# Kernel optimization log

Measured on AMD Instinct MI355X. Metric: run time of the kernel, lower is better.

The kernel has to match this reference:

```python
import jax, jax.numpy as jnp
import numpy as np
from jax import lax

RADII = (0.1, 0.2, 0.4)
NBRS = (16, 32, 64)
PE_DIM = 24
CENTER_PE_DIM = 96
EPS = 1e-5


def sinusoidal_3d(x, dim):
    # x: [..., 3] -> [..., dim]; dim//3 features per axis (half sin, half cos)
    per_axis = dim // 3
    half = per_axis // 2
    freq = jnp.exp(-jnp.log(10000.0) * jnp.arange(half, dtype=x.dtype) / (half - 1))
    ang = x[..., None] * freq                      # [..., 3, half]
    emb = jnp.concatenate([jnp.sin(ang), jnp.cos(ang)], axis=-1)  # [..., 3, per_axis]
    return emb.reshape(x.shape[:-1] + (dim,))


def layer_norm(x, g, b):
    m = jnp.mean(x, axis=-1, keepdims=True)
    v = jnp.var(x, axis=-1, keepdims=True)
    return (x - m) * lax.rsqrt(v + EPS) * g + b


def point_mlp(x, W, b, g, beta, act):
    y = layer_norm(x @ W + b, g, beta)
    return jax.nn.gelu(y, approximate=False) if act else y


def index_points(pts, idx):
    # pts: [B,N,C], idx: [B,...] -> [B,...,C]
    bidx = jnp.arange(pts.shape[0]).reshape((-1,) + (1,) * (idx.ndim - 1))
    return pts[bidx, idx]


def farthest_point_sample(xyz, npoint):
    # xyz: [B,N,3] -> idx [B,npoint]
    N = xyz.shape[1]

    def single(pts):
        def step(carry, _):
            dist, far = carry
            c = pts[far]                                   # [3]
            d = jnp.sum((pts - c) ** 2, axis=-1)           # [N]
            dist = jnp.minimum(dist, d)
            nxt = jnp.argmax(dist).astype(jnp.int32)
            return (dist, nxt), far
        init = (jnp.full((N,), 1e10, pts.dtype), jnp.int32(0))
        _, idxs = lax.scan(step, init, None, length=npoint)
        return idxs

    return jax.vmap(single)(xyz)


def query_ball_point(radius, k, xyz, centers):
    # xyz: [B,N,3], centers: [B,S,3] -> [B,S,k] neighbor indices
    N = xyz.shape[1]
    sqr = jnp.sum((centers[:, :, None, :] - xyz[:, None, :, :]) ** 2, axis=-1)  # [B,S,N]
    gidx = jnp.where(sqr > radius * radius, N, jnp.arange(N)[None, None, :])
    gidx = jnp.sort(gidx, axis=-1)[..., :k]
    first = gidx[..., :1]
    return jnp.where(gidx == N, first, gidx)


def setup_inputs() -> dict:
    key = jax.random.key(0)
    ks = jax.random.split(key, 8)
    B, N, STEM, TOK = 16, 4096, 128, 256
    d_in = STEM + 3 + PE_DIM          # 155
    d_tok_in = STEM + 3 * TOK + CENTER_PE_DIM  # 992
    sc = 0.02
    return {
        "xyz": jax.random.uniform(ks[0], (B, N, 3), dtype=jnp.float32),
        "point_feature": jax.random.normal(ks[1], (B, N, STEM), dtype=jnp.float32) * 0.1,
        "sW1": jax.random.normal(ks[2], (3, d_in, TOK), dtype=jnp.float32) * sc,
        "sb1": jnp.zeros((3, TOK)), "sg1": jnp.ones((3, TOK)), "sbeta1": jnp.zeros((3, TOK)),
        "sW2": jax.random.normal(ks[3], (3, TOK, TOK), dtype=jnp.float32) * sc,
        "sb2": jnp.zeros((3, TOK)), "sg2": jnp.ones((3, TOK)), "sbeta2": jnp.zeros((3, TOK)),
        "tW1": jax.random.normal(ks[4], (d_tok_in, TOK), dtype=jnp.float32) * sc,
        "tb1": jnp.zeros((TOK,)), "tg1": jnp.ones((TOK,)), "tbeta1": jnp.zeros((TOK,)),
        "tW2": jax.random.normal(ks[5], (TOK, TOK), dtype=jnp.float32) * sc,
        "tb2": jnp.zeros((TOK,)), "tg2": jnp.ones((TOK,)), "tbeta2": jnp.zeros((TOK,)),
    }


def reference(xyz, point_feature, sW1, sb1, sg1, sbeta1, sW2, sb2, sg2, sbeta2,
              tW1, tb1, tg1, tbeta1, tW2, tb2, tg2, tbeta2):
    S = 512  # num_patches
    center_idx = farthest_point_sample(xyz, S)            # [B,S]
    patch_center = index_points(xyz, center_idx)          # [B,S,3]
    center_feature = index_points(point_feature, center_idx)  # [B,S,STEM]

    scale_feats = []
    for s, (r, k) in enumerate(zip(RADII, NBRS)):
        nidx = query_ball_point(r, k, xyz, patch_center)  # [B,S,k]
        gxyz = index_points(xyz, nidx)                    # [B,S,k,3]
        gfeat = index_points(point_feature, nidx)         # [B,S,k,STEM]
        rel = gxyz - patch_center[:, :, None, :]
        rel_pe = sinusoidal_3d(rel, PE_DIM)
        gin = jnp.concatenate([gfeat, rel, rel_pe], axis=-1)   # [B,S,k,155]
        h = point_mlp(gin, sW1[s], sb1[s], sg1[s], sbeta1[s], True)
        h = point_mlp(h, sW2[s], sb2[s], sg2[s], sbeta2[s], False)
        scale_feats.append(jnp.max(h, axis=2))            # [B,S,TOK]

    center_pe = sinusoidal_3d(patch_center, CENTER_PE_DIM)    # [B,S,96]
    tok_in = jnp.concatenate([center_feature] + scale_feats + [center_pe], axis=-1)
    tok = point_mlp(tok_in, tW1, tb1, tg1, tbeta1, True)
    tok = point_mlp(tok, tW2, tb2, tg2, tbeta2, False)
    return tok, patch_center
```

## Files before the change

### kernel.cpp

```cpp
#include <hip/hip_runtime.h>
#include <math.h>

#define BATCH 16
#define NPTS  4096
#define NCTR  512
#define STEM  128
#define TOK   256
#define D_IN  155
#define D_TOK 992

typedef short s16x8 __attribute__((ext_vector_type(8)));
typedef float f32x4 __attribute__((ext_vector_type(4)));

static constexpr float FR15c[16] = {
    1.0f, 0.5411695265464638f, 0.2928644487857941f, 0.15848931670188904f,
    0.08576958626508713f, 0.04641588851809502f, 0.02511886507272720f, 0.01359356392547488f,
    0.007356422487646341f, 0.003981071710586548f, 0.002154434798285365f, 0.001165914465673268f,
    0.0006309573450125754f, 0.0003414548910222948f, 0.0001847849769866168f, 0.0001f};

__device__ __forceinline__ unsigned short f2bf(float f) {
    unsigned u = __float_as_uint(f);
    u += 0x7FFF + ((u >> 16) & 1);
    return (unsigned short)(u >> 16);
}
// ... 38 lines not shown
    float t = __builtin_amdgcn_rcpf(fmaf(0.3275911f, a, 1.0f));
    float p = fmaf(1.061405429f, t, -1.453152027f);
    p = fmaf(p, t, 1.421413741f);
    p = fmaf(p, t, -0.284496736f);
    p = fmaf(p, t, 0.254829592f);
    p = p * t;
    float e = __expf(-z * z);
    float y = fmaf(-p, e, 1.0f);
    y = (z < 0.0f) ? -y : y;
    return 0.5f * x * (1.0f + y);
}

__device__ __forceinline__ float sq3(float ax, float ay, float az,
                                     float bx, float by, float bz) {
    float dx = __fsub_rn(ax, bx);
    float dy = __fsub_rn(ay, by);
    float dz = __fsub_rn(az, bz);
    float d = __fmul_rn(dx, dx);
    d = __fadd_rn(d, __fmul_rn(dy, dy));
    d = __fadd_rn(d, __fmul_rn(dz, dz));
    return d;
}

__global__ __launch_bounds__(256) void fps_kernel(const float* __restrict__ xyz,
                                                  int* __restrict__ center_idx,
                                                  float* __restrict__ pc_ws,
                                                  float* __restrict__ pc_out) {
    int b = blockIdx.x;
    int t = threadIdx.x;
    const int w = t >> 6, lane = t & 63;
    const float* X = xyz + (size_t)b * NPTS * 3;
    __shared__ __align__(16) float sxyz[NPTS * 3];
    __shared__ float swv[2][4];
    __shared__ int   swi[2][4];
    __shared__ int   hist[NCTR];
    {
        const float4* src = (const float4*)X;
        float4* dst = (float4*)sxyz;
        for (int i = t; i < NPTS * 3 / 4; i += 256) dst[i] = src[i];
    }
    __syncthreads();
    float px[16], py[16], pz[16], dist[16];
#pragma unroll
    for (int j = 0; j < 16; ++j) {
        int i = t + 256 * j;
        px[j] = sxyz[i * 3 + 0];
        py[j] = sxyz[i * 3 + 1];
        pz[j] = sxyz[i * 3 + 2];
        dist[j] = 1e10f;
    }
    int far = 0;
    for (int s = 0; s < NCTR; ++s) {
        if (t == 0) hist[s] = far;
        float cx = sxyz[far * 3 + 0];
        float cy = sxyz[far * 3 + 1];
        float cz = sxyz[far * 3 + 2];
        float bv = -1.0f;
        int bi = 0;
#pragma unroll
        for (int j = 0; j < 16; ++j) {
            float d = sq3(px[j], py[j], pz[j], cx, cy, cz);
            float nd = fminf(dist[j], d);
            dist[j] = nd;
            if (nd > bv) { bv = nd; bi = t + 256 * j; }
        }
#pragma unroll
        for (int off = 32; off >= 1; off >>= 1) {
            float ov = __shfl_xor(bv, off, 64);
            int   oi = __shfl_xor(bi, off, 64);
            if (ov > bv || (ov == bv && oi < bi)) { bv = ov; bi = oi; }
        }
        const int p = s & 1;
        if (lane == 0) { swv[p][w] = bv; swi[p][w] = bi; }
        __syncthreads();
        bv = swv[p][0]; bi = swi[p][0];
#pragma unroll
        for (int ww = 1; ww < 4; ++ww) {
            float ov = swv[p][ww]; int oi = swi[p][ww];
            if (ov > bv || (ov == bv && oi < bi)) { bv = ov; bi = oi; }
        }
        far = bi;
    }
    __syncthreads();
    for (int s = t; s < NCTR; s += 256) {
        int idx = hist[s];
        center_idx[b * NCTR + s] = idx;
        float cx = sxyz[idx * 3], cy = sxyz[idx * 3 + 1], cz = sxyz[idx * 3 + 2];
        size_t po = (size_t)(b * NCTR + s) * 3;
        pc_ws[po] = cx; pc_ws[po + 1] = cy; pc_ws[po + 2] = cz;
        pc_out[po] = cx; pc_out[po + 1] = cy; pc_out[po + 2] = cz;
    }
}

template <int K>
__global__ __launch_bounds__(256) void ballq_kernel(const float* __restrict__ xyz,
                                                    const float* __restrict__ pc,
                                                    int* __restrict__ nbr,
                                                    float rr) {
    int cid = blockIdx.x * 4 + (threadIdx.x >> 6);
    int lane = threadIdx.x & 63;
    int b = cid >> 9;
    const float* X = xyz + (size_t)b * NPTS * 3;
    float cx = pc[(size_t)cid * 3 + 0];
    float cy = pc[(size_t)cid * 3 + 1];
    float cz = pc[(size_t)cid * 3 + 2];
    int cnt = 0, first = 0;
    bool have_first = false;
    long long base = (long long)cid * K;
    for (int it = 0; it < NPTS / 64; ++it) {
        int i = it * 64 + lane;
        float d = sq3(cx, cy, cz, X[i * 3], X[i * 3 + 1], X[i * 3 + 2]);
        bool ok = d <= rr;
        unsigned long long mask = __ballot(ok);
        if (!have_first && mask) {
            first = it * 64 + (int)__builtin_ctzll(mask);
            have_first = true;
        }
        int pos = cnt + (int)__popcll(mask & ((1ull << lane) - 1ull));
        if (ok && pos < K) nbr[base + pos] = i;
        cnt += (int)__popcll(mask);
        if (cnt >= K) break;
    }
    int fill = cnt < K ? cnt : K;
    for (int j = fill + lane; j < K; j += 64) nbr[base + j] = first;
}

__global__ __launch_bounds__(256) void pack_w(const float* __restrict__ Wbase,
                                              unsigned short* __restrict__ out,
                                              int Kdim, int KS) {
    int s = blockIdx.y;
    const float* W = Wbase + (size_t)s * Kdim * TOK;
    unsigned short* o = out + (size_t)s * 16 * KS * 64 * 16;
    int tid = blockIdx.x * 256 + threadIdx.x;
    if (tid >= 16 * KS * 64) return;
    int lane = tid & 63;
    int frag = tid >> 6;
    int ks = frag % KS;
    int ct = frag / KS;
    int col = ct * 16 + (lane & 15);
    int k0 = ks * 32 + (lane >> 4) * 8;
    unsigned short* hi = o + (size_t)frag * 1024 + lane * 8;
    unsigned short* lo = hi + 512;
#pragma unroll
    for (int j = 0; j < 8; ++j) {
        int k = k0 + j;
        float v = (k < Kdim) ? W[(size_t)k * TOK + col] : 0.0f;
        unsigned short h = f2bf(v);
        hi[j] = h;
        lo[j] = f2bf(v - bf2f(h));
    }
}

template <int K>
__global__ __launch_bounds__(256, 2) void scale_mfma(
    const float* __restrict__ xyz, const float* __restrict__ pf,
    const unsigned short* __restrict__ pk1, const float* __restrict__ b1,
    const float* __restrict__ g1, const float* __restrict__ be1,
    const unsigned short* __restrict__ pk2, const float* __restrict__ b2,
    const float* __restrict__ g2, const float* __restrict__ be2,
    const int* __restrict__ nbr, const float* __restrict__ pc,
    float* __restrict__ outf) {
    __shared__ unsigned int hpk[64][260];
    __shared__ float lnred[4][64][2];
    const int w = threadIdx.x >> 6, l = threadIdx.x & 63;
    const int lg = l >> 4, li = l & 15;
    const int ws4 = 4 * w;

    int nb[4];
    float relx[4], rely[4], relz[4];
#pragma unroll
    for (int rb = 0; rb < 4; ++rb) {
        int row_g = blockIdx.x * 64 + rb * 16 + li;
        int c = (blockIdx.x * 64 + rb * 16) / K;
        int b = c >> 9;
        int n = nbr[row_g];
        nb[rb] = b * NPTS + n;
        const float* X = xyz + (size_t)nb[rb] * 3;
        const float* C = pc + (size_t)c * 3;
        relx[rb] = __fsub_rn(X[0], C[0]);
        rely[rb] = __fsub_rn(X[1], C[1]);
        relz[rb] = __fsub_rn(X[2], C[2]);
    }

    f32x4 acc1[4][4];
#pragma unroll
    for (int rb = 0; rb < 4; ++rb)
#pragma unroll
        for (int ctl = 0; ctl < 4; ++ctl) acc1[rb][ctl] = (f32x4){0.f, 0.f, 0.f, 0.f};

#pragma unroll
    for (int ks = 0; ks < 5; ++ks) {
        s16x8 Bh[4], Bl[4];
#pragma unroll
        for (int ctl = 0; ctl < 4; ++ctl)
            loadB(pk1, (ws4 + ctl) * 5 + ks, l, Bh[ctl], Bl[ctl]);
        s16x8 Ah[4], Al[4];
#pragma unroll
        for (int rb = 0; rb < 4; ++rb) {
            float v[8];
            if (ks < 4) {
                const float* src = pf + (size_t)nb[rb] * STEM + ks * 32 + lg * 8;
                float4 f0 = *(const float4*)src;
                float4 f1 = *(const float4*)(src + 4);
                v[0] = f0.x; v[1] = f0.y; v[2] = f0.z; v[3] = f0.w;
                v[4] = f1.x; v[5] = f1.y; v[6] = f1.z; v[7] = f1.w;
            } else {
#pragma unroll
                for (int j = 0; j < 8; ++j) {
                    int ch = lg * 8 + j;
                    float val = 0.0f;
                    if (ch < 3) {
                        val = (ch == 0) ? relx[rb] : ((ch == 1) ? rely[rb] : relz[rb]);
                    } else if (ch < 27) {
                        int rem = ch - 3;
                        int axis = rem >> 3, r8 = rem & 7;
                        int fi = (r8 < 4) ? r8 : r8 - 4;
                        float fr = (fi == 0) ? 1.0f
                                  : (fi == 1) ? 0.046415888336127795f
                                  : (fi == 2) ? 0.0021544346900318843f : 1e-4f;
                        float rl = (axis == 0) ? relx[rb] : ((axis == 1) ? rely[rb] : relz[rb]);
                        float ang = rl * fr;
                        val = (r8 < 4) ? __sinf(ang) : __cosf(ang);
                    }
                    v[j] = val;
                }
            }
            bsplit8(v, Ah[rb], Al[rb]);
        }
#pragma unroll
        for (int ctl = 0; ctl < 4; ++ctl)
#pragma unroll
            for (int rb = 0; rb < 4; ++rb) {
                acc1[rb][ctl] = __builtin_amdgcn_mfma_f32_16x16x32_bf16(Ah[rb], Bh[ctl], acc1[rb][ctl], 0, 0, 0);
                acc1[rb][ctl] = __builtin_amdgcn_mfma_f32_16x16x32_bf16(Ah[rb], Bl[ctl], acc1[rb][ctl], 0, 0, 0);
                acc1[rb][ctl] = __builtin_amdgcn_mfma_f32_16x16x32_bf16(Al[rb], Bh[ctl], acc1[rb][ctl], 0, 0, 0);
            }
    }

    {
        float b1v[4], g1v[4], be1v[4];
#pragma unroll
        for (int ctl = 0; ctl < 4; ++ctl) {
            int col = w * 64 + ctl * 16 + li;
            b1v[ctl] = b1[col]; g1v[ctl] = g1[col]; be1v[ctl] = be1[col];
        }
#pragma unroll
        for (int rb = 0; rb < 4; ++rb)
#pragma unroll
            for (int reg = 0; reg < 4; ++reg) {
                float s = 0.f, ss = 0.f;
#pragma unroll
                for (int ctl = 0; ctl < 4; ++ctl) {
                    float x = acc1[rb][ctl][reg] + b1v[ctl];
                    s += x; ss = fmaf(x, x, ss);
                }
#pragma unroll
                for (int m = 1; m <= 8; m <<= 1) {
                    s += __shfl_xor(s, m, 64);
                    ss += __shfl_xor(ss, m, 64);
                }
                if (li == 0) {
                    lnred[w][rb * 16 + lg * 4 + reg][0] = s;
                    lnred[w][rb * 16 + lg * 4 + reg][1] = ss;
                }
            }
        __syncthreads();
#pragma unroll
        for (int rb = 0; rb < 4; ++rb)
#pragma unroll
            for (int reg = 0; reg < 4; ++reg) {
                int row = rb * 16 + lg * 4 + reg;
                float s = lnred[0][row][0] + lnred[1][row][0] + lnred[2][row][0] + lnred[3][row][0];
                float ss = lnred[0][row][1] + lnred[1][row][1] + lnred[2][row][1] + lnred[3][row][1];
                float mean = s * (1.0f / 256.0f);
                float var = ss * (1.0f / 256.0f) - mean * mean;
                float rs = rsqrtf(var + 1e-5f);
#pragma unroll
                for (int ctl = 0; ctl < 4; ++ctl) {
                    float x = acc1[rb][ctl][reg] + b1v[ctl];
                    acc1[rb][ctl][reg] = gelu_exact((x - mean) * rs * g1v[ctl] + be1v[ctl]);
                }
            }
    }

#pragma unroll
    for (int rb = 0; rb < 4; ++rb)
#pragma unroll
        for (int ctl = 0; ctl < 4; ++ctl) {
            unsigned w0, w1, w2, w3;
            pkpair(acc1[rb][ctl][0], acc1[rb][ctl][1], w0, w1);
            pkpair(acc1[rb][ctl][2], acc1[rb][ctl][3], w2, w3);
            int r0 = rb * 16 + lg * 4;
            int kc = w * 64 + ctl * 16 + li;
            hpk[r0 + 0][kc] = w0; hpk[r0 + 1][kc] = w1;
            hpk[r0 + 2][kc] = w2; hpk[r0 + 3][kc] = w3;
        }
    __syncthreads();

    f32x4 acc2[4][4];
#pragma unroll
    for (int rb = 0; rb < 4; ++rb)
#pragma unroll
        for (int ctl = 0; ctl < 4; ++ctl) acc2[rb][ctl] = (f32x4){0.f, 0.f, 0.f, 0.f};

#pragma unroll
    for (int q = 0; q < 8; ++q) {
        s16x8 Bh[4], Bl[4];
#pragma unroll
        for (int ctl = 0; ctl < 4; ++ctl)
            loadB(pk2, (ws4 + ctl) * 8 + q, l, Bh[ctl], Bl[ctl]);
#pragma unroll
        for (int rb = 0; rb < 4; ++rb) {
            const unsigned int* hp = &hpk[rb * 16 + li][q * 32 + lg * 8];
            int4 xa = *(const int4*)hp;
            int4 xb = *(const int4*)(hp + 4);
            unsigned x[8] = {(unsigned)xa.x, (unsigned)xa.y, (unsigned)xa.z, (unsigned)xa.w,
                             (unsigned)xb.x, (unsigned)xb.y, (unsigned)xb.z, (unsigned)xb.w};
            union { s16x8 s; unsigned w[4]; } H, L;
#pragma unroll
            for (int p = 0; p < 4; ++p) {
                H.w[p] = (x[2 * p] >> 16) | (x[2 * p + 1] & 0xffff0000u);
                L.w[p] = (x[2 * p] & 0xffffu) | (x[2 * p + 1] << 16);
            }
#pragma unroll
            for (int ctl = 0; ctl < 4; ++ctl) {
                acc2[rb][ctl] = __builtin_amdgcn_mfma_f32_16x16x32_bf16(H.s, Bh[ctl], acc2[rb][ctl], 0, 0, 0);
                acc2[rb][ctl] = __builtin_amdgcn_mfma_f32_16x16x32_bf16(H.s, Bl[ctl], acc2[rb][ctl], 0, 0, 0);
                acc2[rb][ctl] = __builtin_amdgcn_mfma_f32_16x16x32_bf16(L.s, Bh[ctl], acc2[rb][ctl], 0, 0, 0);
            }
        }
    }

    float b2v[4], g2v[4], be2v[4];
#pragma unroll
    for (int ctl = 0; ctl < 4; ++ctl) {
        int col = w * 64 + ctl * 16 + li;
        b2v[ctl] = b2[col]; g2v[ctl] = g2[col]; be2v[ctl] = be2[col];
    }
#pragma unroll
    for (int rb = 0; rb < 4; ++rb)
#pragma unroll
        for (int reg = 0; reg < 4; ++reg) {
            float s = 0.f, ss = 0.f;
#pragma unroll
            for (int ctl = 0; ctl < 4; ++ctl) {
                float x = acc2[rb][ctl][reg] + b2v[ctl];
                s += x; ss = fmaf(x, x, ss);
            }
#pragma unroll
            for (int m = 1; m <= 8; m <<= 1) {
                s += __shfl_xor(s, m, 64);
                ss += __shfl_xor(ss, m, 64);
            }
            if (li == 0) {
                lnred[w][rb * 16 + lg * 4 + reg][0] = s;
                lnred[w][rb * 16 + lg * 4 + reg][1] = ss;
            }
        }
    __syncthreads();
#pragma unroll
    for (int rb = 0; rb < 4; ++rb)
#pragma unroll
        for (int reg = 0; reg < 4; ++reg) {
            int row = rb * 16 + lg * 4 + reg;
            float s = lnred[0][row][0] + lnred[1][row][0] + lnred[2][row][0] + lnred[3][row][0];
            float ss = lnred[0][row][1] + lnred[1][row][1] + lnred[2][row][1] + lnred[3][row][1];
            float mean = s * (1.0f / 256.0f);
            float var = ss * (1.0f / 256.0f) - mean * mean;
            float rs = rsqrtf(var + 1e-5f);
#pragma unroll
            for (int ctl = 0; ctl < 4; ++ctl) {
                float x = acc2[rb][ctl][reg] + b2v[ctl];
                acc2[rb][ctl][reg] = (x - mean) * rs * g2v[ctl] + be2v[ctl];
            }
        }

    const int CPB = 64 / K;
    const int RBC = K / 16;
#pragma unroll
    for (int cg = 0; cg < CPB; ++cg)
#pragma unroll
        for (int ctl = 0; ctl < 4; ++ctl) {
            float mx = -3.4e38f;
#pragma unroll
            for (int rbl = 0; rbl < RBC; ++rbl) {
                int rb = cg * RBC + rbl;
#pragma unroll
                for (int reg = 0; reg < 4; ++reg) mx = fmaxf(mx, acc2[rb][ctl][reg]);
            }
            mx = fmaxf(mx, __shfl_xor(mx, 16, 64));
            mx = fmaxf(mx, __shfl_xor(mx, 32, 64));
            if (lg == 0)
                outf[(size_t)(blockIdx.x * CPB + cg) * TOK + w * 64 + ctl * 16 + li] = mx;
        }
}

__global__ __launch_bounds__(256, 2) void token_mfma(
    const float* __restrict__ pf, const int* __restrict__ center_idx,
    const float* __restrict__ pc, const float* __restrict__ sf0,
    const float* __restrict__ sf1, const float* __restrict__ sf2,
    const unsigned short* __restrict__ pk1, const float* __restrict__ b1,
    const float* __restrict__ g1, const float* __restrict__ be1,
    const unsigned short* __restrict__ pk2, const float* __restrict__ b2,
    const float* __restrict__ g2, const float* __restrict__ be2,
    float* __restrict__ out) {
    __shared__ unsigned int hpk[32][260];
    __shared__ float lnred[4][32][2];
    const int w = threadIdx.x >> 6, l = threadIdx.x & 63;
    const int lg = l >> 4, li = l & 15;
    const int ws4 = 4 * w;
    const int rowbase = blockIdx.x * 32;

    int rowg[2];
    const float* pfc[2];
    float pcx[2], pcy[2], pcz[2];
#pragma unroll
    for (int rb = 0; rb < 2; ++rb) {
        int row = rowbase + rb * 16 + li;
        rowg[rb] = row;
        int b = row >> 9;
        int cidx = center_idx[row];
        pfc[rb] = pf + ((size_t)b * NPTS + cidx) * STEM;
        pcx[rb] = pc[(size_t)row * 3 + 0];
        pcy[rb] = pc[(size_t)row * 3 + 1];
        pcz[rb] = pc[(size_t)row * 3 + 2];
    }

    f32x4 acc1[2][4];
#pragma unroll
    for (int rb = 0; rb < 2; ++rb)
#pragma unroll
        for (int ctl = 0; ctl < 4; ++ctl) acc1[rb][ctl] = (f32x4){0.f, 0.f, 0.f, 0.f};

#pragma unroll 2
    for (int ks = 0; ks < 31; ++ks) {
        s16x8 Bh[4], Bl[4];
#pragma unroll
        for (int ctl = 0; ctl < 4; ++ctl)
            loadB(pk1, (ws4 + ctl) * 31 + ks, l, Bh[ctl], Bl[ctl]);
        s16x8 Ah[2], Al[2];
#pragma unroll
        for (int rb = 0; rb < 2; ++rb) {
            float v[8];
            if (ks < 28) {
                const float* src;
                if (ks < 4)       src = pfc[rb] + ks * 32 + lg * 8;
                else if (ks < 12) src = sf0 + (size_t)rowg[rb] * TOK + (ks - 4) * 32 + lg * 8;
                else if (ks < 20) src = sf1 + (size_t)rowg[rb] * TOK + (ks - 12) * 32 + lg * 8;
                else              src = sf2 + (size_t)rowg[rb] * TOK + (ks - 20) * 32 + lg * 8;
                float4 f0 = *(const float4*)src;
                float4 f1 = *(const float4*)(src + 4);
                v[0] = f0.x; v[1] = f0.y; v[2] = f0.z; v[3] = f0.w;
                v[4] = f1.x; v[5] = f1.y; v[6] = f1.z; v[7] = f1.w;
            } else {
                float c = (ks == 28) ? pcx[rb] : ((ks == 29) ? pcy[rb] : pcz[rb]);
#pragma unroll
                for (int j = 0; j < 8; ++j) {
                    float fr = (lg & 1) ? FR15c[8 + j] : FR15c[j];
                    float ang = c * fr;
                    v[j] = (lg < 2) ? __sinf(ang) : __cosf(ang);
                }
            }
            bsplit8(v, Ah[rb], Al[rb]);
        }
#pragma unroll
        for (int ctl = 0; ctl < 4; ++ctl)
#pragma unroll
            for (int rb = 0; rb < 2; ++rb) {
                acc1[rb][ctl] = __builtin_amdgcn_mfma_f32_16x16x32_bf16(Ah[rb], Bh[ctl], acc1[rb][ctl], 0, 0, 0);
                acc1[rb][ctl] = __builtin_amdgcn_mfma_f32_16x16x32_bf16(Ah[rb], Bl[ctl], acc1[rb][ctl], 0, 0, 0);
                acc1[rb][ctl] = __builtin_amdgcn_mfma_f32_16x16x32_bf16(Al[rb], Bh[ctl], acc1[rb][ctl], 0, 0, 0);
            }
    }

    {
        float b1v[4], g1v[4], be1v[4];
#pragma unroll
        for (int ctl = 0; ctl < 4; ++ctl) {
            int col = w * 64 + ctl * 16 + li;
            b1v[ctl] = b1[col]; g1v[ctl] = g1[col]; be1v[ctl] = be1[col];
        }
#pragma unroll
        for (int rb = 0; rb < 2; ++rb)
#pragma unroll
            for (int reg = 0; reg < 4; ++reg) {
                float s = 0.f, ss = 0.f;
#pragma unroll
                for (int ctl = 0; ctl < 4; ++ctl) {
                    float x = acc1[rb][ctl][reg] + b1v[ctl];
                    s += x; ss = fmaf(x, x, ss);
                }
#pragma unroll
                for (int m = 1; m <= 8; m <<= 1) {
                    s += __shfl_xor(s, m, 64);
                    ss += __shfl_xor(ss, m, 64);
                }
                if (li == 0) {
                    lnred[w][rb * 16 + lg * 4 + reg][0] = s;
                    lnred[w][rb * 16 + lg * 4 + reg][1] = ss;
                }
            }
        __syncthreads();
#pragma unroll
        for (int rb = 0; rb < 2; ++rb)
#pragma unroll
            for (int reg = 0; reg < 4; ++reg) {
                int row = rb * 16 + lg * 4 + reg;
                float s = lnred[0][row][0] + lnred[1][row][0] + lnred[2][row][0] + lnred[3][row][0];
                float ss = lnred[0][row][1] + lnred[1][row][1] + lnred[2][row][1] + lnred[3][row][1];
                float mean = s * (1.0f / 256.0f);
                float var = ss * (1.0f / 256.0f) - mean * mean;
                float rs = rsqrtf(var + 1e-5f);
#pragma unroll
                for (int ctl = 0; ctl < 4; ++ctl) {
                    float x = acc1[rb][ctl][reg] + b1v[ctl];
                    acc1[rb][ctl][reg] = gelu_exact((x - mean) * rs * g1v[ctl] + be1v[ctl]);
                }
            }
    }

#pragma unroll
    for (int rb = 0; rb < 2; ++rb)
#pragma unroll
        for (int ctl = 0; ctl < 4; ++ctl) {
            unsigned w0, w1, w2, w3;
            pkpair(acc1[rb][ctl][0], acc1[rb][ctl][1], w0, w1);
            pkpair(acc1[rb][ctl][2], acc1[rb][ctl][3], w2, w3);
            int r0 = rb * 16 + lg * 4;
            int kc = w * 64 + ctl * 16 + li;
            hpk[r0 + 0][kc] = w0; hpk[r0 + 1][kc] = w1;
            hpk[r0 + 2][kc] = w2; hpk[r0 + 3][kc] = w3;
        }
    __syncthreads();

    f32x4 acc2[2][4];
#pragma unroll
    for (int rb = 0; rb < 2; ++rb)
#pragma unroll
        for (int ctl = 0; ctl < 4; ++ctl) acc2[rb][ctl] = (f32x4){0.f, 0.f, 0.f, 0.f};
#pragma unroll
    for (int q = 0; q < 8; ++q) {
        s16x8 Bh[4], Bl[4];
#pragma unroll
        for (int ctl = 0; ctl < 4; ++ctl)
            loadB(pk2, (ws4 + ctl) * 8 + q, l, Bh[ctl], Bl[ctl]);
#pragma unroll
        for (int rb = 0; rb < 2; ++rb) {
            const unsigned int* hp = &hpk[rb * 16 + li][q * 32 + lg * 8];
            int4 xa = *(const int4*)hp;
            int4 xb = *(const int4*)(hp + 4);
            unsigned x[8] = {(unsigned)xa.x, (unsigned)xa.y, (unsigned)xa.z, (unsigned)xa.w,
                             (unsigned)xb.x, (unsigned)xb.y, (unsigned)xb.z, (unsigned)xb.w};
            union { s16x8 s; unsigned w[4]; } H, L;
#pragma unroll
            for (int p = 0; p < 4; ++p) {
                H.w[p] = (x[2 * p] >> 16) | (x[2 * p + 1] & 0xffff0000u);
                L.w[p] = (x[2 * p] & 0xffffu) | (x[2 * p + 1] << 16);
            }
#pragma unroll
            for (int ctl = 0; ctl < 4; ++ctl) {
                acc2[rb][ctl] = __builtin_amdgcn_mfma_f32_16x16x32_bf16(H.s, Bh[ctl], acc2[rb][ctl], 0, 0, 0);
                acc2[rb][ctl] = __builtin_amdgcn_mfma_f32_16x16x32_bf16(H.s, Bl[ctl], acc2[rb][ctl], 0, 0, 0);
                acc2[rb][ctl] = __builtin_amdgcn_mfma_f32_16x16x32_bf16(L.s, Bh[ctl], acc2[rb][ctl], 0, 0, 0);
            }
        }
    }

    float b2v[4], g2v[4], be2v[4];
#pragma unroll
    for (int ctl = 0; ctl < 4; ++ctl) {
        int col = w * 64 + ctl * 16 + li;
        b2v[ctl] = b2[col]; g2v[ctl] = g2[col]; be2v[ctl] = be2[col];
    }
#pragma unroll
    for (int rb = 0; rb < 2; ++rb)
#pragma unroll
        for (int reg = 0; reg < 4; ++reg) {
            float s = 0.f, ss = 0.f;
#pragma unroll
            for (int ctl = 0; ctl < 4; ++ctl) {
                float x = acc2[rb][ctl][reg] + b2v[ctl];
                s += x; ss = fmaf(x, x, ss);
            }
#pragma unroll
            for (int m = 1; m <= 8; m <<= 1) {
                s += __shfl_xor(s, m, 64);
                ss += __shfl_xor(ss, m, 64);
            }
            if (li == 0) {
                lnred[w][rb * 16 + lg * 4 + reg][0] = s;
                lnred[w][rb * 16 + lg * 4 + reg][1] = ss;
            }
        }
    __syncthreads();
#pragma unroll
    for (int rb = 0; rb < 2; ++rb)
#pragma unroll
        for (int reg = 0; reg < 4; ++reg) {
            int row = rb * 16 + lg * 4 + reg;
            float s = lnred[0][row][0] + lnred[1][row][0] + lnred[2][row][0] + lnred[3][row][0];
            float ss = lnred[0][row][1] + lnred[1][row][1] + lnred[2][row][1] + lnred[3][row][1];
            float mean = s * (1.0f / 256.0f);
            float var = ss * (1.0f / 256.0f) - mean * mean;
            float rs = rsqrtf(var + 1e-5f);
#pragma unroll
            for (int ctl = 0; ctl < 4; ++ctl) {
                float x = acc2[rb][ctl][reg] + b2v[ctl];
                float v = (x - mean) * rs * g2v[ctl] + be2v[ctl];
                out[(size_t)(rowbase + row) * TOK + w * 64 + ctl * 16 + li] = v;
            }
        }
}

extern "C" void kernel_launch(void* const* d_in, const int* in_sizes, int n_in,
                              void* d_out, int out_size, void* d_ws, size_t ws_size,
                              hipStream_t stream) {
    const float* xyz  = (const float*)d_in[0];
    const float* pf   = (const float*)d_in[1];
    const float* sW1  = (const float*)d_in[2];
    const float* sb1  = (const float*)d_in[3];
    const float* sg1  = (const float*)d_in[4];
    const float* sbe1 = (const float*)d_in[5];
    const float* sW2  = (const float*)d_in[6];
    const float* sb2  = (const float*)d_in[7];
    const float* sg2  = (const float*)d_in[8];
    const float* sbe2 = (const float*)d_in[9];
    const float* tW1  = (const float*)d_in[10];
    const float* tb1  = (const float*)d_in[11];
    const float* tg1  = (const float*)d_in[12];
    const float* tbe1 = (const float*)d_in[13];
    const float* tW2  = (const float*)d_in[14];
    const float* tb2  = (const float*)d_in[15];
    const float* tg2  = (const float*)d_in[16];
    const float* tbe2 = (const float*)d_in[17];

    float* out_tok = (float*)d_out;
    float* out_pc  = out_tok + (size_t)BATCH * NCTR * TOK;

    char* ws = (char*)d_ws;
    int* center_idx = (int*)ws;   ws += (size_t)BATCH * NCTR * 4;
    float* pc_ws    = (float*)ws; ws += (size_t)BATCH * NCTR * 3 * 4;
    int* nbr0       = (int*)ws;   ws += (size_t)BATCH * NCTR * 16 * 4;
    int* nbr1       = (int*)ws;   ws += (size_t)BATCH * NCTR * 32 * 4;
    int* nbr2       = (int*)ws;   ws += (size_t)BATCH * NCTR * 64 * 4;
    float* sf0      = (float*)ws; ws += (size_t)BATCH * NCTR * TOK * 4;
    float* sf1      = (float*)ws; ws += (size_t)BATCH * NCTR * TOK * 4;
    float* sf2      = (float*)ws; ws += (size_t)BATCH * NCTR * TOK * 4;
    const size_t PK1_S  = 16 * 5 * 64 * 16;
    const size_t PK2_S  = 16 * 8 * 64 * 16;
    const size_t PKT1_S = 16 * 31 * 64 * 16;
    const size_t PKT2_S = 16 * 8 * 64 * 16;
    unsigned short* pkW1 = (unsigned short*)ws; ws += 3 * PK1_S * 2;
    unsigned short* pkW2 = (unsigned short*)ws; ws += 3 * PK2_S * 2;
    unsigned short* pkT1 = (unsigned short*)ws; ws += PKT1_S * 2;
    unsigned short* pkT2 = (unsigned short*)ws; ws += PKT2_S * 2;

    {
        dim3 gp1((16 * 5 * 64 + 255) / 256, 3);
        pack_w<<<gp1, 256, 0, stream>>>(sW1, pkW1, D_IN, 5);
        dim3 gp2((16 * 8 * 64 + 255) / 256, 3);
        pack_w<<<gp2, 256, 0, stream>>>(sW2, pkW2, TOK, 8);
        dim3 gpt1((16 * 31 * 64 + 255) / 256, 1);
        pack_w<<<gpt1, 256, 0, stream>>>(tW1, pkT1, D_TOK, 31);
        dim3 gpt2((16 * 8 * 64 + 255) / 256, 1);
        pack_w<<<gpt2, 256, 0, stream>>>(tW2, pkT2, TOK, 8);
    }

    fps_kernel<<<BATCH, 256, 0, stream>>>(xyz, center_idx, pc_ws, out_pc);

    ballq_kernel<16><<<BATCH * NCTR / 4, 256, 0, stream>>>(xyz, pc_ws, nbr0, (float)(0.1 * 0.1));
    ballq_kernel<32><<<BATCH * NCTR / 4, 256, 0, stream>>>(xyz, pc_ws, nbr1, (float)(0.2 * 0.2));
    ballq_kernel<64><<<BATCH * NCTR / 4, 256, 0, stream>>>(xyz, pc_ws, nbr2, (float)(0.4 * 0.4));

    scale_mfma<16><<<(BATCH * NCTR * 16) / 64, 256, 0, stream>>>(
        xyz, pf, pkW1 + 0 * PK1_S, sb1 + 0 * TOK, sg1 + 0 * TOK, sbe1 + 0 * TOK,
        pkW2 + 0 * PK2_S, sb2 + 0 * TOK, sg2 + 0 * TOK, sbe2 + 0 * TOK,
        nbr0, pc_ws, sf0);
    scale_mfma<32><<<(BATCH * NCTR * 32) / 64, 256, 0, stream>>>(
        xyz, pf, pkW1 + 1 * PK1_S, sb1 + 1 * TOK, sg1 + 1 * TOK, sbe1 + 1 * TOK,
        pkW2 + 1 * PK2_S, sb2 + 1 * TOK, sg2 + 1 * TOK, sbe2 + 1 * TOK,
        nbr1, pc_ws, sf1);
    scale_mfma<64><<<(BATCH * NCTR * 64) / 64, 256, 0, stream>>>(
        xyz, pf, pkW1 + 2 * PK1_S, sb1 + 2 * TOK, sg1 + 2 * TOK, sbe1 + 2 * TOK,
        pkW2 + 2 * PK2_S, sb2 + 2 * TOK, sg2 + 2 * TOK, sbe2 + 2 * TOK,
        nbr2, pc_ws, sf2);

    token_mfma<<<(BATCH * NCTR) / 32, 256, 0, stream>>>(
        pf, center_idx, pc_ws, sf0, sf1, sf2,
        pkT1, tb1, tg1, tbe1, pkT2, tb2, tg2, tbe2, out_tok);
}
```

Baseline: 1.634 ms.

## Split second GEMM into half-row passes, swizzle LDS, shrink token blocks

The scale kernel now runs its second GEMM and LayerNorm in two passes of 32 rows each. This halves the LDS staging buffer and the acc2 register footprint, and the staging buffer uses an XOR swizzle instead of row padding. Max-pooling is done per pass, with a running max carried across passes for K=64. Launch bounds rise to 3 blocks per CU to raise occupancy. The token kernel drops to 16 rows per block with double the grid, trading weight reuse for lower register and LDS use and more parallelism.

```diff
diff --git a/kernel.cpp b/kernel.cpp
--- a/kernel.cpp
+++ b/kernel.cpp
@@ -214,7 +214,7 @@
 }
 
 template <int K>
-__global__ __launch_bounds__(256, 2) void scale_mfma(
+__global__ __launch_bounds__(256, 3) void scale_mfma(
     const float* __restrict__ xyz, const float* __restrict__ pf,
     const unsigned short* __restrict__ pk1, const float* __restrict__ b1,
     const float* __restrict__ g1, const float* __restrict__ be1,
@@ -222,7 +222,7 @@
     const float* __restrict__ g2, const float* __restrict__ be2,
     const int* __restrict__ nbr, const float* __restrict__ pc,
     float* __restrict__ outf) {
-    __shared__ unsigned int hpk[64][260];
+    __shared__ unsigned int hpk[32 * 256];
     __shared__ float lnred[4][64][2];
     const int w = threadIdx.x >> 6, l = threadIdx.x & 63;
     const int lg = l >> 4, li = l & 15;
@@ -345,119 +345,160 @@
             }
     }
 
-#pragma unroll
-    for (int rb = 0; rb < 4; ++rb)
-#pragma unroll
-        for (int ctl = 0; ctl < 4; ++ctl) {
-            unsigned w0, w1, w2, w3;
-            pkpair(acc1[rb][ctl][0], acc1[rb][ctl][1], w0, w1);
-            pkpair(acc1[rb][ctl][2], acc1[rb][ctl][3], w2, w3);
-            int r0 = rb * 16 + lg * 4;
-            int kc = w * 64 + ctl * 16 + li;
-            hpk[r0 + 0][kc] = w0; hpk[r0 + 1][kc] = w1;
-            hpk[r0 + 2][kc] = w2; hpk[r0 + 3][kc] = w3;
-        }
-    __syncthreads();
-
-    f32x4 acc2[4][4];
-#pragma unroll
-    for (int rb = 0; rb < 4; ++rb)
-#pragma unroll
-        for (int ctl = 0; ctl < 4; ++ctl) acc2[rb][ctl] = (f32x4){0.f, 0.f, 0.f, 0.f};
-
-#pragma unroll
-    for (int q = 0; q < 8; ++q) {
-        s16x8 Bh[4], Bl[4];
-#pragma unroll
-        for (int ctl = 0; ctl < 4; ++ctl)
-            loadB(pk2, (ws4 + ctl) * 8 + q, l, Bh[ctl], Bl[ctl]);
-#pragma unroll
-        for (int rb = 0; rb < 4; ++rb) {
-            const unsigned int* hp = &hpk[rb * 16 + li][q * 32 + lg * 8];
-            int4 xa = *(const int4*)hp;
-            int4 xb = *(const int4*)(hp + 4);
-            unsigned x[8] = {(unsigned)xa.x, (unsigned)xa.y, (unsigned)xa.z, (unsigned)xa.w,
-                             (unsigned)xb.x, (unsigned)xb.y, (unsigned)xb.z, (unsigned)xb.w};
-            union { s16x8 s; unsigned w[4]; } H, L;
-#pragma unroll
-            for (int p = 0; p < 4; ++p) {
-                H.w[p] = (x[2 * p] >> 16) | (x[2 * p + 1] & 0xffff0000u);
-                L.w[p] = (x[2 * p] & 0xffffu) | (x[2 * p + 1] << 16);
-            }
-#pragma unroll
-            for (int ctl = 0; ctl < 4; ++ctl) {
-                acc2[rb][ctl] = __builtin_amdgcn_mfma_f32_16x16x32_bf16(H.s, Bh[ctl], acc2[rb][ctl], 0, 0, 0);
-                acc2[rb][ctl] = __builtin_amdgcn_mfma_f32_16x16x32_bf16(H.s, Bl[ctl], acc2[rb][ctl], 0, 0, 0);
-                acc2[rb][ctl] = __builtin_amdgcn_mfma_f32_16x16x32_bf16(L.s, Bh[ctl], acc2[rb][ctl], 0, 0, 0);
-            }
-        }
-    }
-
     float b2v[4], g2v[4], be2v[4];
 #pragma unroll
     for (int ctl = 0; ctl < 4; ++ctl) {
         int col = w * 64 + ctl * 16 + li;
         b2v[ctl] = b2[col]; g2v[ctl] = g2[col]; be2v[ctl] = be2[col];
     }
-#pragma unroll
-    for (int rb = 0; rb < 4; ++rb)
-#pragma unroll
-        for (int reg = 0; reg < 4; ++reg) {
-            float s = 0.f, ss = 0.f;
+    float mx64[4];
+#pragma unroll
+    for (int ctl = 0; ctl < 4; ++ctl) mx64[ctl] = -3.4e38f;
+
+#pragma unroll
+    for (int p = 0; p < 2; ++p) {
+#pragma unroll
+        for (int rbl = 0; rbl < 2; ++rbl) {
+            const int rb = 2 * p + rbl;
 #pragma unroll
             for (int ctl = 0; ctl < 4; ++ctl) {
-                float x = acc2[rb][ctl][reg] + b2v[ctl];
-                s += x; ss = fmaf(x, x, ss);
-            }
-#pragma unroll
-            for (int m = 1; m <= 8; m <<= 1) {
-                s += __shfl_xor(s, m, 64);
-                ss += __shfl_xor(ss, m, 64);
-            }
-            if (li == 0) {
-                lnred[w][rb * 16 + lg * 4 + reg][0] = s;
-                lnred[w][rb * 16 + lg * 4 + reg][1] = ss;
-            }
-        }
-    __syncthreads();
-#pragma unroll
-    for (int rb = 0; rb < 4; ++rb)
-#pragma unroll
-        for (int reg = 0; reg < 4; ++reg) {
-            int row = rb * 16 + lg * 4 + reg;
-            float s = lnred[0][row][0] + lnred[1][row][0] + lnred[2][row][0] + lnred[3][row][0];
-            float ss = lnred[0][row][1] + lnred[1][row][1] + lnred[2][row][1] + lnred[3][row][1];
-            float mean = s * (1.0f / 256.0f);
-            float var = ss * (1.0f / 256.0f) - mean * mean;
-            float rs = rsqrtf(var + 1e-5f);
+                unsigned w0, w1, w2, w3;
+                pkpair(acc1[rb][ctl][0], acc1[rb][ctl][1], w0, w1);
+                pkpair(acc1[rb][ctl][2], acc1[rb][ctl][3], w2, w3);
+                const int lr0 = rbl * 16 + lg * 4;
+                const int kc = w * 64 + ctl * 16 + li;
+                hpk[(lr0 + 0) * 256 + (kc ^ (((lr0 + 0) & 7) << 2))] = w0;
+                hpk[(lr0 + 1) * 256 + (kc ^ (((lr0 + 1) & 7) << 2))] = w1;
+                hpk[(lr0 + 2) * 256 + (kc ^ (((lr0 + 2) & 7) << 2))] = w2;
+                hpk[(lr0 + 3) * 256 + (kc ^ (((lr0 + 3) & 7) << 2))] = w3;
+            }
+        }
+        __syncthreads();
+
+        f32x4 acc2[2][4];
+#pragma unroll
+        for (int rbl = 0; rbl < 2; ++rbl)
+#pragma unroll
+            for (int ctl = 0; ctl < 4; ++ctl) acc2[rbl][ctl] = (f32x4){0.f, 0.f, 0.f, 0.f};
+
+#pragma unroll
+        for (int q = 0; q < 8; ++q) {
+            s16x8 Bh[4], Bl[4];
+#pragma unroll
+            for (int ctl = 0; ctl < 4; ++ctl)
+                loadB(pk2, (ws4 + ctl) * 8 + q, l, Bh[ctl], Bl[ctl]);
+#pragma unroll
+            for (int rbl = 0; rbl < 2; ++rbl) {
+                const int lr = rbl * 16 + li;
+                const int sw = (lr & 7) << 2;
+                const unsigned* base = hpk + lr * 256;
+                int4 xa = *(const int4*)(base + ((q * 32 + lg * 8) ^ sw));
+                int4 xb = *(const int4*)(base + ((q * 32 + lg * 8 + 4) ^ sw));
+                unsigned x[8] = {(unsigned)xa.x, (unsigned)xa.y, (unsigned)xa.z, (unsigned)xa.w,
+                                 (unsigned)xb.x, (unsigned)xb.y, (unsigned)xb.z, (unsigned)xb.w};
+                union { s16x8 s; unsigned w[4]; } H, L;
+#pragma unroll
+                for (int pp = 0; pp < 4; ++pp) {
+                    H.w[pp] = (x[2 * pp] >> 16) | (x[2 * pp + 1] & 0xffff0000u);
+                    L.w[pp] = (x[2 * pp] & 0xffffu) | (x[2 * pp + 1] << 16);
+                }
+#pragma unroll
+                for (int ctl = 0; ctl < 4; ++ctl) {
+                    acc2[rbl][ctl] = __builtin_amdgcn_mfma_f32_16x16x32_bf16(H.s, Bh[ctl], acc2[rbl][ctl], 0, 0, 0);
+                    acc2[rbl][ctl] = __builtin_amdgcn_mfma_f32_16x16x32_bf16(H.s, Bl[ctl], acc2[rbl][ctl], 0, 0, 0);
+                    acc2[rbl][ctl] = __builtin_amdgcn_mfma_f32_16x16x32_bf16(L.s, Bh[ctl], acc2[rbl][ctl], 0, 0, 0);
+                }
+            }
+        }
+
+#pragma unroll
+        for (int rbl = 0; rbl < 2; ++rbl)
+#pragma unroll
+            for (int reg = 0; reg < 4; ++reg) {
+                float s = 0.f, ss = 0.f;
+#pragma unroll
+                for (int ctl = 0; ctl < 4; ++ctl) {
+                    float x = acc2[rbl][ctl][reg] + b2v[ctl];
+                    s += x; ss = fmaf(x, x, ss);
+                }
+#pragma unroll
+                for (int m = 1; m <= 8; m <<= 1) {
+                    s += __shfl_xor(s, m, 64);
+                    ss += __shfl_xor(ss, m, 64);
+                }
+                if (li == 0) {
+                    lnred[w][rbl * 16 + lg * 4 + reg][0] = s;
+                    lnred[w][rbl * 16 + lg * 4 + reg][1] = ss;
+                }
+            }
+        __syncthreads();
+
+#pragma unroll
+        for (int rbl = 0; rbl < 2; ++rbl)
+#pragma unroll
+            for (int reg = 0; reg < 4; ++reg) {
+                int row = rbl * 16 + lg * 4 + reg;
+                float s = lnred[0][row][0] + lnred[1][row][0] + lnred[2][row][0] + lnred[3][row][0];
+                float ss = lnred[0][row][1] + lnred[1][row][1] + lnred[2][row][1] + lnred[3][row][1];
+                float mean = s * (1.0f / 256.0f);
+                float var = ss * (1.0f / 256.0f) - mean * mean;
+                float rs = rsqrtf(var + 1e-5f);
+#pragma unroll
+                for (int ctl = 0; ctl < 4; ++ctl) {
+                    float x = acc2[rbl][ctl][reg] + b2v[ctl];
+                    acc2[rbl][ctl][reg] = (x - mean) * rs * g2v[ctl] + be2v[ctl];
+                }
+            }
+
+        if (K == 64) {
+#pragma unroll
+            for (int rbl = 0; rbl < 2; ++rbl)
+#pragma unroll
+                for (int ctl = 0; ctl < 4; ++ctl)
+#pragma unroll
+                    for (int reg = 0; reg < 4; ++reg)
+                        mx64[ctl] = fmaxf(mx64[ctl], acc2[rbl][ctl][reg]);
+        } else if (K == 32) {
 #pragma unroll
             for (int ctl = 0; ctl < 4; ++ctl) {
-                float x = acc2[rb][ctl][reg] + b2v[ctl];
-                acc2[rb][ctl][reg] = (x - mean) * rs * g2v[ctl] + be2v[ctl];
-            }
-        }
-
-    const int CPB = 64 / K;
-    const int RBC = K / 16;
-#pragma unroll
-    for (int cg = 0; cg < CPB; ++cg)
+                float mx = -3.4e38f;
+#pragma unroll
+                for (int rbl = 0; rbl < 2; ++rbl)
+#pragma unroll
+                    for (int reg = 0; reg < 4; ++reg) mx = fmaxf(mx, acc2[rbl][ctl][reg]);
+                mx = fmaxf(mx, __shfl_xor(mx, 16, 64));
+                mx = fmaxf(mx, __shfl_xor(mx, 32, 64));
+                if (lg == 0)
+                    outf[(size_t)(blockIdx.x * 2 + p) * TOK + w * 64 + ctl * 16 + li] = mx;
+            }
+        } else {
+#pragma unroll
+            for (int rbl = 0; rbl < 2; ++rbl)
+#pragma unroll
+                for (int ctl = 0; ctl < 4; ++ctl) {
+                    float mx = -3.4e38f;
+#pragma unroll
+                    for (int reg = 0; reg < 4; ++reg) mx = fmaxf(mx, acc2[rbl][ctl][reg]);
+                    mx = fmaxf(mx, __shfl_xor(mx, 16, 64));
+                    mx = fmaxf(mx, __shfl_xor(mx, 32, 64));
+                    if (lg == 0)
+                        outf[(size_t)(blockIdx.x * 4 + 2 * p + rbl) * TOK + w * 64 + ctl * 16 + li] = mx;
+                }
+        }
+    }
+    if (K == 64) {
 #pragma unroll
         for (int ctl = 0; ctl < 4; ++ctl) {
-            float mx = -3.4e38f;
-#pragma unroll
-            for (int rbl = 0; rbl < RBC; ++rbl) {
-                int rb = cg * RBC + rbl;
-#pragma unroll
-                for (int reg = 0; reg < 4; ++reg) mx = fmaxf(mx, acc2[rb][ctl][reg]);
-            }
+            float mx = mx64[ctl];
             mx = fmaxf(mx, __shfl_xor(mx, 16, 64));
             mx = fmaxf(mx, __shfl_xor(mx, 32, 64));
             if (lg == 0)
-                outf[(size_t)(blockIdx.x * CPB + cg) * TOK + w * 64 + ctl * 16 + li] = mx;
-        }
-}
-
-__global__ __launch_bounds__(256, 2) void token_mfma(
+                outf[(size_t)blockIdx.x * TOK + w * 64 + ctl * 16 + li] = mx;
+        }
+    }
+}
+
+__global__ __launch_bounds__(256, 3) void token_mfma(
     const float* __restrict__ pf, const int* __restrict__ center_idx,
     const float* __restrict__ pc, const float* __restrict__ sf0,
     const float* __restrict__ sf1, const float* __restrict__ sf2,
@@ -466,33 +507,24 @@
     const unsigned short* __restrict__ pk2, const float* __restrict__ b2,
     const float* __restrict__ g2, const float* __restrict__ be2,
     float* __restrict__ out) {
-    __shared__ unsigned int hpk[32][260];
-    __shared__ float lnred[4][32][2];
+    __shared__ unsigned int hpk[16][260];
+    __shared__ float lnred[4][16][2];
     const int w = threadIdx.x >> 6, l = threadIdx.x & 63;
     const int lg = l >> 4, li = l & 15;
     const int ws4 = 4 * w;
-    const int rowbase = blockIdx.x * 32;
-
-    int rowg[2];
-    const float* pfc[2];
-    float pcx[2], pcy[2], pcz[2];
-#pragma unroll
-    for (int rb = 0; rb < 2; ++rb) {
-        int row = rowbase + rb * 16 + li;
-        rowg[rb] = row;
-        int b = row >> 9;
-        int cidx = center_idx[row];
-        pfc[rb] = pf + ((size_t)b * NPTS + cidx) * STEM;
-        pcx[rb] = pc[(size_t)row * 3 + 0];
-        pcy[rb] = pc[(size_t)row * 3 + 1];
-        pcz[rb] = pc[(size_t)row * 3 + 2];
-    }
-
-    f32x4 acc1[2][4];
-#pragma unroll
-    for (int rb = 0; rb < 2; ++rb)
-#pragma unroll
-        for (int ctl = 0; ctl < 4; ++ctl) acc1[rb][ctl] = (f32x4){0.f, 0.f, 0.f, 0.f};
+    const int rowbase = blockIdx.x * 16;
+
+    const int rowg = rowbase + li;
+    const int bb = rowg >> 9;
+    const int cidx = center_idx[rowg];
+    const float* pfc = pf + ((size_t)bb * NPTS + cidx) * STEM;
+    const float pcx = pc[(size_t)rowg * 3 + 0];
+    const float pcy = pc[(size_t)rowg * 3 + 1];
+    const float pcz = pc[(size_t)rowg * 3 + 2];
+
+    f32x4 acc1[4];
+#pragma unroll
+    for (int ctl = 0; ctl < 4; ++ctl) acc1[ctl] = (f32x4){0.f, 0.f, 0.f, 0.f};
 
 #pragma unroll 2
     for (int ks = 0; ks < 31; ++ks) {
@@ -500,22 +532,21 @@
 #pragma unroll
         for (int ctl = 0; ctl < 4; ++ctl)
             loadB(pk1, (ws4 + ctl) * 31 + ks, l, Bh[ctl], Bl[ctl]);
-        s16x8 Ah[2], Al[2];
-#pragma unroll
-        for (int rb = 0; rb < 2; ++rb) {
+        s16x8 Ah, Al;
+        {
             float v[8];
             if (ks < 28) {
                 const float* src;
-                if (ks < 4)       src = pfc[rb] + ks * 32 + lg * 8;
-                else if (ks < 12) src = sf0 + (size_t)rowg[rb] * TOK + (ks - 4) * 32 + lg * 8;
-                else if (ks < 20) src = sf1 + (size_t)rowg[rb] * TOK + (ks - 12) * 32 + lg * 8;
-                else              src = sf2 + (size_t)rowg[rb] * TOK + (ks - 20) * 32 + lg * 8;
+                if (ks < 4)       src = pfc + ks * 32 + lg * 8;
+                else if (ks < 12) src = sf0 + (size_t)rowg * TOK + (ks - 4) * 32 + lg * 8;
+                else if (ks < 20) src = sf1 + (size_t)rowg * TOK + (ks - 12) * 32 + lg * 8;
+                else              src = sf2 + (size_t)rowg * TOK + (ks - 20) * 32 + lg * 8;
                 float4 f0 = *(const float4*)src;
                 float4 f1 = *(const float4*)(src + 4);
                 v[0] = f0.x; v[1] = f0.y; v[2] = f0.z; v[3] = f0.w;
                 v[4] = f1.x; v[5] = f1.y; v[6] = f1.z; v[7] = f1.w;
             } else {
-                float c = (ks == 28) ? pcx[rb] : ((ks == 29) ? pcy[rb] : pcz[rb]);
+                float c = (ks == 28) ? pcx : ((ks == 29) ? pcy : pcz);
 #pragma unroll
                 for (int j = 0; j < 8; ++j) {
                     float fr = (lg & 1) ? FR15c[8 + j] : FR15c[j];
@@ -523,16 +554,14 @@
                     v[j] = (lg < 2) ? __sinf(ang) : __cosf(ang);
                 }
             }
-            bsplit8(v, Ah[rb], Al[rb]);
-        }
-#pragma unroll
-        for (int ctl = 0; ctl < 4; ++ctl)
-#pragma unroll
-            for (int rb = 0; rb < 2; ++rb) {
-                acc1[rb][ctl] = __builtin_amdgcn_mfma_f32_16x16x32_bf16(Ah[rb], Bh[ctl], acc1[rb][ctl], 0, 0, 0);
-                acc1[rb][ctl] = __builtin_amdgcn_mfma_f32_16x16x32_bf16(Ah[rb], Bl[ctl], acc1[rb][ctl], 0, 0, 0);
-                acc1[rb][ctl] = __builtin_amdgcn_mfma_f32_16x16x32_bf16(Al[rb], Bh[ctl], acc1[rb][ctl], 0, 0, 0);
-            }
+            bsplit8(v, Ah, Al);
+        }
+#pragma unroll
+        for (int ctl = 0; ctl < 4; ++ctl) {
+            acc1[ctl] = __builtin_amdgcn_mfma_f32_16x16x32_bf16(Ah, Bh[ctl], acc1[ctl], 0, 0, 0);
+            acc1[ctl] = __builtin_amdgcn_mfma_f32_16x16x32_bf16(Ah, Bl[ctl], acc1[ctl], 0, 0, 0);
+            acc1[ctl] = __builtin_amdgcn_mfma_f32_16x16x32_bf16(Al, Bh[ctl], acc1[ctl], 0, 0, 0);
+        }
     }
 
     {
@@ -543,105 +572,11 @@
             b1v[ctl] = b1[col]; g1v[ctl] = g1[col]; be1v[ctl] = be1[col];
         }
 #pragma unroll
-        for (int rb = 0; rb < 2; ++rb)
-#pragma unroll
-            for (int reg = 0; reg < 4; ++reg) {
-                float s = 0.f, ss = 0.f;
-#pragma unroll
-                for (int ctl = 0; ctl < 4; ++ctl) {
-                    float x = acc1[rb][ctl][reg] + b1v[ctl];
-                    s += x; ss = fmaf(x, x, ss);
-                }
-#pragma unroll
-                for (int m = 1; m <= 8; m <<= 1) {
-                    s += __shfl_xor(s, m, 64);
-                    ss += __shfl_xor(ss, m, 64);
-                }
-                if (li == 0) {
-                    lnred[w][rb * 16 + lg * 4 + reg][0] = s;
-                    lnred[w][rb * 16 + lg * 4 + reg][1] = ss;
-                }
-            }
-        __syncthreads();
-#pragma unroll
-        for (int rb = 0; rb < 2; ++rb)
-#pragma unroll
-            for (int reg = 0; reg < 4; ++reg) {
-                int row = rb * 16 + lg * 4 + reg;
-                float s = lnred[0][row][0] + lnred[1][row][0] + lnred[2][row][0] + lnred[3][row][0];
-                float ss = lnred[0][row][1] + lnred[1][row][1] + lnred[2][row][1] + lnred[3][row][1];
-                float mean = s * (1.0f / 256.0f);
-                float var = ss * (1.0f / 256.0f) - mean * mean;
-                float rs = rsqrtf(var + 1e-5f);
-#pragma unroll
-                for (int ctl = 0; ctl < 4; ++ctl) {
-                    float x = acc1[rb][ctl][reg] + b1v[ctl];
-                    acc1[rb][ctl][reg] = gelu_exact((x - mean) * rs * g1v[ctl] + be1v[ctl]);
-                }
-            }
-    }
-
-#pragma unroll
-    for (int rb = 0; rb < 2; ++rb)
-#pragma unroll
-        for (int ctl = 0; ctl < 4; ++ctl) {
-            unsigned w0, w1, w2, w3;
-            pkpair(acc1[rb][ctl][0], acc1[rb][ctl][1], w0, w1);
-            pkpair(acc1[rb][ctl][2], acc1[rb][ctl][3], w2, w3);
-            int r0 = rb * 16 + lg * 4;
-            int kc = w * 64 + ctl * 16 + li;
-            hpk[r0 + 0][kc] = w0; hpk[r0 + 1][kc] = w1;
-            hpk[r0 + 2][kc] = w2; hpk[r0 + 3][kc] = w3;
-        }
-    __syncthreads();
-
-    f32x4 acc2[2][4];
-#pragma unroll
-    for (int rb = 0; rb < 2; ++rb)
-#pragma unroll
-        for (int ctl = 0; ctl < 4; ++ctl) acc2[rb][ctl] = (f32x4){0.f, 0.f, 0.f, 0.f};
-#pragma unroll
-    for (int q = 0; q < 8; ++q) {
-        s16x8 Bh[4], Bl[4];
-#pragma unroll
-        for (int ctl = 0; ctl < 4; ++ctl)
-            loadB(pk2, (ws4 + ctl) * 8 + q, l, Bh[ctl], Bl[ctl]);
-#pragma unroll
-        for (int rb = 0; rb < 2; ++rb) {
-            const unsigned int* hp = &hpk[rb * 16 + li][q * 32 + lg * 8];
-            int4 xa = *(const int4*)hp;
-            int4 xb = *(const int4*)(hp + 4);
-            unsigned x[8] = {(unsigned)xa.x, (unsigned)xa.y, (unsigned)xa.z, (unsigned)xa.w,
-                             (unsigned)xb.x, (unsigned)xb.y, (unsigned)xb.z, (unsigned)xb.w};
-            union { s16x8 s; unsigned w[4]; } H, L;
-#pragma unroll
-            for (int p = 0; p < 4; ++p) {
-                H.w[p] = (x[2 * p] >> 16) | (x[2 * p + 1] & 0xffff0000u);
-                L.w[p] = (x[2 * p] & 0xffffu) | (x[2 * p + 1] << 16);
-            }
-#pragma unroll
-            for (int ctl = 0; ctl < 4; ++ctl) {
-                acc2[rb][ctl] = __builtin_amdgcn_mfma_f32_16x16x32_bf16(H.s, Bh[ctl], acc2[rb][ctl], 0, 0, 0);
-                acc2[rb][ctl] = __builtin_amdgcn_mfma_f32_16x16x32_bf16(H.s, Bl[ctl], acc2[rb][ctl], 0, 0, 0);
-                acc2[rb][ctl] = __builtin_amdgcn_mfma_f32_16x16x32_bf16(L.s, Bh[ctl], acc2[rb][ctl], 0, 0, 0);
-            }
-        }
-    }
-
-    float b2v[4], g2v[4], be2v[4];
-#pragma unroll
-    for (int ctl = 0; ctl < 4; ++ctl) {
-        int col = w * 64 + ctl * 16 + li;
-        b2v[ctl] = b2[col]; g2v[ctl] = g2[col]; be2v[ctl] = be2[col];
-    }
-#pragma unroll
-    for (int rb = 0; rb < 2; ++rb)
-#pragma unroll
         for (int reg = 0; reg < 4; ++reg) {
             float s = 0.f, ss = 0.f;
 #pragma unroll
             for (int ctl = 0; ctl < 4; ++ctl) {
-                float x = acc2[rb][ctl][reg] + b2v[ctl];
+                float x = acc1[ctl][reg] + b1v[ctl];
                 s += x; ss = fmaf(x, x, ss);
             }
 #pragma unroll
@@ -650,16 +585,14 @@
                 ss += __shfl_xor(ss, m, 64);
             }
             if (li == 0) {
-                lnred[w][rb * 16 + lg * 4 + reg][0] = s;
-                lnred[w][rb * 16 + lg * 4 + reg][1] = ss;
-            }
-        }
-    __syncthreads();
-#pragma unroll
-    for (int rb = 0; rb < 2; ++rb)
+                lnred[w][lg * 4 + reg][0] = s;
+                lnred[w][lg * 4 + reg][1] = ss;
+            }
+        }
+        __syncthreads();
 #pragma unroll
         for (int reg = 0; reg < 4; ++reg) {
-            int row = rb * 16 + lg * 4 + reg;
+            int row = lg * 4 + reg;
             float s = lnred[0][row][0] + lnred[1][row][0] + lnred[2][row][0] + lnred[3][row][0];
             float ss = lnred[0][row][1] + lnred[1][row][1] + lnred[2][row][1] + lnred[3][row][1];
             float mean = s * (1.0f / 256.0f);
@@ -667,11 +600,92 @@
             float rs = rsqrtf(var + 1e-5f);
 #pragma unroll
             for (int ctl = 0; ctl < 4; ++ctl) {
-                float x = acc2[rb][ctl][reg] + b2v[ctl];
-                float v = (x - mean) * rs * g2v[ctl] + be2v[ctl];
-                out[(size_t)(rowbase + row) * TOK + w * 64 + ctl * 16 + li] = v;
-            }
-        }
+                float x = acc1[ctl][reg] + b1v[ctl];
+                acc1[ctl][reg] = gelu_exact((x - mean) * rs * g1v[ctl] + be1v[ctl]);
+            }
+        }
+    }
+
+#pragma unroll
+    for (int ctl = 0; ctl < 4; ++ctl) {
+        unsigned w0, w1, w2, w3;
+        pkpair(acc1[ctl][0], acc1[ctl][1], w0, w1);
+        pkpair(acc1[ctl][2], acc1[ctl][3], w2, w3);
+        int r0 = lg * 4;
+        int kc = w * 64 + ctl * 16 + li;
+        hpk[r0 + 0][kc] = w0; hpk[r0 + 1][kc] = w1;
+        hpk[r0 + 2][kc] = w2; hpk[r0 + 3][kc] = w3;
+    }
+    __syncthreads();
+
+    f32x4 acc2[4];
+#pragma unroll
+    for (int ctl = 0; ctl < 4; ++ctl) acc2[ctl] = (f32x4){0.f, 0.f, 0.f, 0.f};
+#pragma unroll
+    for (int q = 0; q < 8; ++q) {
+        s16x8 Bh[4], Bl[4];
+#pragma unroll
+        for (int ctl = 0; ctl < 4; ++ctl)
+            loadB(pk2, (ws4 + ctl) * 8 + q, l, Bh[ctl], Bl[ctl]);
+        const unsigned int* hp = &hpk[li][q * 32 + lg * 8];
+        int4 xa = *(const int4*)hp;
+        int4 xb = *(const int4*)(hp + 4);
+        unsigned x[8] = {(unsigned)xa.x, (unsigned)xa.y, (unsigned)xa.z, (unsigned)xa.w,
+                         (unsigned)xb.x, (unsigned)xb.y, (unsigned)xb.z, (unsigned)xb.w};
+        union { s16x8 s; unsigned w[4]; } H, L;
+#pragma unroll
+        for (int pp = 0; pp < 4; ++pp) {
+            H.w[pp] = (x[2 * pp] >> 16) | (x[2 * pp + 1] & 0xffff0000u);
+            L.w[pp] = (x[2 * pp] & 0xffffu) | (x[2 * pp + 1] << 16);
+        }
+#pragma unroll
+        for (int ctl = 0; ctl < 4; ++ctl) {
+            acc2[ctl] = __builtin_amdgcn_mfma_f32_16x16x32_bf16(H.s, Bh[ctl], acc2[ctl], 0, 0, 0);
+            acc2[ctl] = __builtin_amdgcn_mfma_f32_16x16x32_bf16(H.s, Bl[ctl], acc2[ctl], 0, 0, 0);
+            acc2[ctl] = __builtin_amdgcn_mfma_f32_16x16x32_bf16(L.s, Bh[ctl], acc2[ctl], 0, 0, 0);
+        }
+    }
+
+    float b2v[4], g2v[4], be2v[4];
+#pragma unroll
+    for (int ctl = 0; ctl < 4; ++ctl) {
+        int col = w * 64 + ctl * 16 + li;
+        b2v[ctl] = b2[col]; g2v[ctl] = g2[col]; be2v[ctl] = be2[col];
+    }
+#pragma unroll
+    for (int reg = 0; reg < 4; ++reg) {
+        float s = 0.f, ss = 0.f;
+#pragma unroll
+        for (int ctl = 0; ctl < 4; ++ctl) {
+            float x = acc2[ctl][reg] + b2v[ctl];
+            s += x; ss = fmaf(x, x, ss);
+        }
+#pragma unroll
+        for (int m = 1; m <= 8; m <<= 1) {
+            s += __shfl_xor(s, m, 64);
+            ss += __shfl_xor(ss, m, 64);
+        }
+        if (li == 0) {
+            lnred[w][lg * 4 + reg][0] = s;
+            lnred[w][lg * 4 + reg][1] = ss;
+        }
+    }
+    __syncthreads();
+#pragma unroll
+    for (int reg = 0; reg < 4; ++reg) {
+        int row = lg * 4 + reg;
+        float s = lnred[0][row][0] + lnred[1][row][0] + lnred[2][row][0] + lnred[3][row][0];
+        float ss = lnred[0][row][1] + lnred[1][row][1] + lnred[2][row][1] + lnred[3][row][1];
+        float mean = s * (1.0f / 256.0f);
+        float var = ss * (1.0f / 256.0f) - mean * mean;
+        float rs = rsqrtf(var + 1e-5f);
+#pragma unroll
+        for (int ctl = 0; ctl < 4; ++ctl) {
+            float x = acc2[ctl][reg] + b2v[ctl];
+            float v = (x - mean) * rs * g2v[ctl] + be2v[ctl];
+            out[(size_t)(rowbase + row) * TOK + w * 64 + ctl * 16 + li] = v;
+        }
+    }
 }
 
 extern "C" void kernel_launch(void* const* d_in, const int* in_sizes, int n_in,
@@ -747,7 +761,7 @@
         pkW2 + 2 * PK2_S, sb2 + 2 * TOK, sg2 + 2 * TOK, sbe2 + 2 * TOK,
         nbr2, pc_ws, sf2);
 
-    token_mfma<<<(BATCH * NCTR) / 32, 256, 0, stream>>>(
+    token_mfma<<<(BATCH * NCTR) / 16, 256, 0, stream>>>(
         pf, center_idx, pc_ws, sf0, sf1, sf2,
         pkT1, tb1, tg1, tbe1, pkT2, tb2, tg2, tbe2, out_tok);
 }
```

Result: slower. 2.594 ms (+58.7%).
